# Optimization experiments

Measured on AMD Instinct MI355X. Metric: run time of the kernel, lower is better.

## Reference

```python
import jax, jax.numpy as jnp
import numpy as np

B, C, H, W = 16, 128, 32, 32
D, K = 64, 8192
BN_EPS = 1e-5
KLD_SCALE = 10.0
COMMIT = 0.25


def setup_inputs() -> dict:
    key = jax.random.key(0)
    ks = jax.random.split(key, 4)
    return {
        "z": jax.random.normal(ks[0], (B, C, H, W), dtype=jnp.float32),
        "proj_w": jax.random.normal(ks[1], (D, C), dtype=jnp.float32) * (1.0 / np.sqrt(C)),
        "proj_b": jax.random.normal(ks[2], (D,), dtype=jnp.float32) * 0.01,
        "gamma": jnp.ones((D,), dtype=jnp.float32),
        "beta": jnp.zeros((D,), dtype=jnp.float32),
        "running_mean": jnp.zeros((D,), dtype=jnp.float32),
        "running_var": jnp.ones((D,), dtype=jnp.float32),
        "embed": jax.random.normal(ks[3], (K, D), dtype=jnp.float32) * 0.1,
    }


def reference(z, proj_w, proj_b, gamma, beta, running_mean, running_var, embed):
    sg = jax.lax.stop_gradient
    b, c, h, w = z.shape
    # 1x1 conv projection: [B,C,H,W] -> [B,D,H,W]
    x = jnp.einsum('bchw,dc->bdhw', z, proj_w) + proj_b[None, :, None, None]
    # BatchNorm2d (inference mode: running stats)
    scale = gamma * jax.lax.rsqrt(running_var + BN_EPS)
    x = x * scale[None, :, None, None] + (beta - running_mean * scale)[None, :, None, None]
    # NCHW -> NHWC, flatten to [N, D]
    z_e = jnp.transpose(x, (0, 2, 3, 1))
    flat = z_e.reshape(-1, z_e.shape[-1])  # [N, D]
    # pairwise squared distances [N, K]
    dist = (jnp.sum(flat * flat, axis=1, keepdims=True)
            - 2.0 * flat @ embed.T
            + jnp.sum(embed * embed, axis=1)[None, :])
    ind = jnp.argmax(-dist, axis=1).reshape(b, h, w)  # [B,H,W]
    z_q = embed[ind]  # [B,H,W,D] codebook gather
    diff = KLD_SCALE * (COMMIT * jnp.mean((sg(z_q) - z_e) ** 2)
                        + jnp.mean((z_q - sg(z_e)) ** 2))
    z_q_st = z_e + sg(z_q - z_e)  # straight-through
    return jnp.transpose(z_q_st, (0, 3, 1, 2)), diff, ind
```

## Files before the change

### kernel.cpp

```cpp
#include <hip/hip_runtime.h>
#include <math.h>

#define B_   16
#define C_   128
#define H_   32
#define W_   32
#define D_   64
#define K_   8192
#define HW_  (H_*W_)
#define N_   (B_*HW_)

#define CS      16
#define CPB     (K_/CS)
#define CHUNK   128
#define NCH     (CPB/CHUNK)
#define ROWS_PB 256
#define MARGIN  0.12f
#define CAND_CAP 32

typedef short v8s __attribute__((ext_vector_type(8)));
typedef float v4f __attribute__((ext_vector_type(4)));

__device__ __forceinline__ short f2bf(float f) {
    union { float fv; unsigned u; } cv; cv.fv = f;
    unsigned u = cv.u;
    unsigned rnd = ((u >> 16) & 1u) + 0x7fffu;
    return (short)((u + rnd) >> 16);
}

#define GLOAD_LDS16(gp, lp) __builtin_amdgcn_global_load_lds( \
    (const __attribute__((address_space(1))) unsigned int*)(gp), \
    (__attribute__((address_space(3))) unsigned int*)(lp), 16, 0, 0)

__device__ __forceinline__ float exact_score(const float4* __restrict__ zr,
                                             const float* __restrict__ embed,
                                             float h, int k)
{
    const float4* ep = (const float4*)(embed + (size_t)k * D_);
    float sa = 0.f, sb = 0.f;
    #pragma unroll
    for (int d4 = 0; d4 < 16; d4 += 2) {
        float4 ea = ep[d4], eb = ep[d4 + 1];
        sa += ea.x*zr[d4].x + ea.y*zr[d4].y + ea.z*zr[d4].z + ea.w*zr[d4].w;
        sb += eb.x*zr[d4+1].x + eb.y*zr[d4+1].y + eb.z*zr[d4+1].z + eb.w*zr[d4+1].w;
    }
    return (sa + sb) - h;
}

__global__ __launch_bounds__(256) void k_proj(
    const float* __restrict__ z, const float* __restrict__ pw,
    const float* __restrict__ pb, const float* __restrict__ gamma,
    const float* __restrict__ beta, const float* __restrict__ rmean,
    const float* __restrict__ rvar, float* __restrict__ ze,
    short* __restrict__ zbf)
{
    __shared__ float zt[64][132];
    __shared__ float wl[64][132];
    const int tid = threadIdx.x;
    const int n0  = blockIdx.x * 64;
    const int b   = n0 / HW_;
    const int hw0 = n0 % HW_;
    const float* zb = z + (size_t)b * C_ * HW_ + hw0;

    #pragma unroll
    for (int it = 0; it < 32; ++it) {
        int flat = tid + 256 * it;
        int c = flat >> 6, p = flat & 63;
        zt[p][c] = zb[c * HW_ + p];
    }
    #pragma unroll
    for (int it = 0; it < 32; ++it) {
        int flat = tid + 256 * it;
        int d = flat >> 7, c = flat & 127;
        wl[d][c] = pw[d * C_ + c];
    }
    __syncthreads();

    const int tp = tid & 15;
    const int td = tid >> 4;
    float acc[4][4] = {};
    #pragma unroll
    for (int c4 = 0; c4 < 32; ++c4) {
        float4 zv[4], wv[4];
        #pragma unroll
        for (int i = 0; i < 4; ++i) zv[i] = *(const float4*)&zt[4*tp + i][4*c4];
        #pragma unroll
        for (int j = 0; j < 4; ++j) wv[j] = *(const float4*)&wl[4*td + j][4*c4];
        #pragma unroll
        for (int i = 0; i < 4; ++i)
            #pragma unroll
            for (int j = 0; j < 4; ++j)
                acc[i][j] += zv[i].x*wv[j].x + zv[i].y*wv[j].y
                           + zv[i].z*wv[j].z + zv[i].w*wv[j].w;
    }

    float sc[4], bi[4];
    #pragma unroll
    for (int j = 0; j < 4; ++j) {
        int d = 4*td + j;
        float s = gamma[d] / sqrtf(rvar[d] + 1e-5f);
        sc[j] = s;
        bi[j] = pb[d] * s + beta[d] - rmean[d] * s;
    }
    #pragma unroll
    for (int i = 0; i < 4; ++i) {
        int n = n0 + 4*tp + i;
        float4 o;
        o.x = acc[i][0]*sc[0] + bi[0];
        o.y = acc[i][1]*sc[1] + bi[1];
        o.z = acc[i][2]*sc[2] + bi[2];
        o.w = acc[i][3]*sc[3] + bi[3];
        *(float4*)&ze[(size_t)n * D_ + 4*td] = o;
        short4 ob;
        ob.x = f2bf(o.x); ob.y = f2bf(o.y); ob.z = f2bf(o.z); ob.w = f2bf(o.w);
        *(short4*)&zbf[(size_t)n * D_ + 4*td] = ob;
    }
}

__global__ __launch_bounds__(256) void k_prep(const float* __restrict__ e,
                                              float* __restrict__ hn,
                                              short* __restrict__ ebs)
{
    int t = blockIdx.x * 256 + threadIdx.x;
    float4 v = ((const float4*)e)[t];
    float s = v.x*v.x + v.y*v.y + v.z*v.z + v.w*v.w;
    s += __shfl_xor(s, 1);
    s += __shfl_xor(s, 2);
    s += __shfl_xor(s, 4);
    s += __shfl_xor(s, 8);
    if ((threadIdx.x & 15) == 0) hn[t >> 4] = 0.5f * s;

    const int k = t >> 4, p = t & 15;
    if (p < 8) {
        const int j = p ^ (k & 7);
        const float* src = e + (size_t)k * D_ + j * 8;
        v8s o;
        #pragma unroll
        for (int i = 0; i < 8; ++i) o[i] = f2bf(src[i]);
        *(v8s*)(ebs + (size_t)k * D_ + p * 8) = o;
    }
}

template<bool PUSH>
__global__ __launch_bounds__(256) void k_sweep(
    const short* __restrict__ zbf, const short* __restrict__ ebs,
    const float* __restrict__ hn, float* __restrict__ pbest,
    const float* __restrict__ Vm, int* __restrict__ cnt,
    int* __restrict__ cand)
{
    __shared__ short eb[2][CHUNK * 64];
    __shared__ float hl[2][CHUNK];
    const int tid  = threadIdx.x;
    const int lane = tid & 63;
    const int wv   = tid >> 6;
    const int q    = lane >> 4;
    const int l15  = lane & 15;
    const int m8   = l15 & 7;
    const int rowBase = blockIdx.x * ROWS_PB + wv * 64;
    const int code0   = blockIdx.y * CPB;

    v8s A[4][2];
    #pragma unroll
    for (int rt = 0; rt < 4; ++rt)
        #pragma unroll
        for (int f = 0; f < 2; ++f)
            A[rt][f] = *(const v8s*)(zbf + (size_t)(rowBase + rt*16 + l15) * D_
                                      + f*32 + q*8);

    float best[4][4];
    float vm[4][4];
    if (PUSH) {
        #pragma unroll
        for (int rt = 0; rt < 4; ++rt)
            #pragma unroll
            for (int r = 0; r < 4; ++r)
                vm[rt][r] = Vm[rowBase + rt*16 + q*4 + r];
    } else {
        #pragma unroll
        for (int rt = 0; rt < 4; ++rt)
            #pragma unroll
            for (int r = 0; r < 4; ++r) best[rt][r] = -INFINITY;
    }

    const int rb0 = l15 * 64 + ((q ^ m8) * 8);
    const int rb1 = l15 * 64 + (((q ^ m8) ^ 4) * 8);

    const char* srcBase = (const char*)(ebs + (size_t)code0 * 64);
    #define STAGE(b, ch) do {                                              \
        const char* s_ = srcBase + (size_t)(ch) * (CHUNK * 128);           \
        char* l_ = (char*)&eb[(b)][0];                                     \
        _Pragma("unroll")                                                  \
        for (int i_ = 0; i_ < 4; ++i_) {                                   \
            int seg_ = (wv * 4 + i_) * 1024 + lane * 16;                   \
            GLOAD_LDS16(s_ + seg_, l_ + seg_);                             \
        }                                                                  \
        if (tid < CHUNK) hl[(b)][tid] = hn[code0 + (ch) * CHUNK + tid];    \
    } while (0)

    STAGE(0, 0);
    __syncthreads();

    #pragma unroll 1
    for (int ch = 0; ch < NCH; ++ch) {
        const int buf = ch & 1;
        if (ch + 1 < NCH) STAGE(buf ^ 1, ch + 1);
        const int c0 = code0 + ch * CHUNK;
        const short* ep = &eb[buf][0];

        #pragma unroll
        for (int t = 0; t < CHUNK / 16; ++t) {
            v8s B0 = *(const v8s*)(ep + rb0 + t * 1024);
            v8s B1 = *(const v8s*)(ep + rb1 + t * 1024);
            const float mh = -hl[buf][t * 16 + l15];
            #pragma unroll
            for (int rt = 0; rt < 4; ++rt) {
                v4f c = {mh, mh, mh, mh};
                c = __builtin_amdgcn_mfma_f32_16x16x32_bf16(A[rt][0], B0, c, 0, 0, 0);
                c = __builtin_amdgcn_mfma_f32_16x16x32_bf16(A[rt][1], B1, c, 0, 0, 0);
                if (!PUSH) {
                    #pragma unroll
                    for (int r = 0; r < 4; ++r) best[rt][r] = fmaxf(best[rt][r], c[r]);
                } else {
                    bool a0 = c[0] > vm[rt][0];
                    bool a1 = c[1] > vm[rt][1];
                    bool a2 = c[2] > vm[rt][2];
                    bool a3 = c[3] > vm[rt][3];
                    if (a0 | a1 | a2 | a3) {
                        const int code = c0 + t * 16 + l15;
                        const int row0 = rowBase + rt*16 + q*4;
                        #pragma unroll
                        for (int r = 0; r < 4; ++r) {
                            if (c[r] > vm[rt][r]) {
                                int s = atomicAdd(&cnt[row0 + r], 1);
                                if (s < CAND_CAP) cand[(row0 + r) * CAND_CAP + s] = code;
                            }
                        }
                    }
                }
            }
        }
        __syncthreads();
    }
    #undef STAGE

    if (!PUSH) {
        #pragma unroll
        for (int rt = 0; rt < 4; ++rt)
            #pragma unroll
            for (int r = 0; r < 4; ++r) {
                float v = best[rt][r];
                v = fmaxf(v, __shfl_xor(v, 1));
                v = fmaxf(v, __shfl_xor(v, 2));
                v = fmaxf(v, __shfl_xor(v, 4));
                v = fmaxf(v, __shfl_xor(v, 8));
                if (l15 == 0)
                    pbest[(size_t)blockIdx.y * N_ + rowBase + rt*16 + q*4 + r] = v;
            }
    }
}

__global__ __launch_bounds__(256) void k_comb(const float* __restrict__ pbest,
                                              float* __restrict__ Vm,
                                              int* __restrict__ cnt)
{
    int n = blockIdx.x * 256 + threadIdx.x;
    float v = -INFINITY;
    #pragma unroll
    for (int s = 0; s < CS; ++s) v = fmaxf(v, pbest[(size_t)s * N_ + n]);
    Vm[n] = v - MARGIN;
    cnt[n] = 0;
}

__global__ __launch_bounds__(64) void k_pick(
    const int* __restrict__ cnt, const int* __restrict__ cand,
    const float* __restrict__ embed, const float* __restrict__ hn,
    const float* __restrict__ ze, float* __restrict__ out0,
    float* __restrict__ outIdx, float* __restrict__ bsum)
{
    const int tid = threadIdx.x;
    const int n   = blockIdx.x * 64 + tid;

    float4 zr[16];
    const float4* zp = (const float4*)(ze + (size_t)n * D_);
    #pragma unroll
    for (int i = 0; i < 16; ++i) zr[i] = zp[i];

    const int m = cnt[n];
    float best = -INFINITY;
    int   bidx = 0x7fffffff;
    if (m > CAND_CAP) {
        for (int k = 0; k < K_; ++k) {
            float s = exact_score(zr, embed, hn[k], k);
            if (s > best) { best = s; bidx = k; }
        }
    } else {
        for (int i = 0; i < m; ++i) {
            int k = cand[n * CAND_CAP + i];
            float s = exact_score(zr, embed, hn[k], k);
            if (s > best || (s == best && k < bidx)) { best = s; bidx = k; }
        }
    }
    if (bidx == 0x7fffffff) bidx = 0;
    outIdx[n] = (float)bidx;

    const float4* eq = (const float4*)(embed + (size_t)bidx * D_);
    const int b = n >> 10, hw = n & 1023;
    float* o = out0 + (size_t)b * (D_ * HW_) + hw;

    float local = 0.f;
    #pragma unroll
    for (int d4 = 0; d4 < 16; ++d4) {
        float4 e = eq[d4], zv = zr[d4];
        float dx = e.x - zv.x, dy = e.y - zv.y, dz = e.z - zv.z, dw = e.w - zv.w;
        local += dx*dx + dy*dy + dz*dz + dw*dw;
        o[(4*d4 + 0) * HW_] = e.x;
        o[(4*d4 + 1) * HW_] = e.y;
        o[(4*d4 + 2) * HW_] = e.z;
        o[(4*d4 + 3) * HW_] = e.w;
    }

    local += __shfl_xor(local, 1);
    local += __shfl_xor(local, 2);
    local += __shfl_xor(local, 4);
    local += __shfl_xor(local, 8);
    local += __shfl_xor(local, 16);
    local += __shfl_xor(local, 32);
    if (tid == 0) bsum[blockIdx.x] = local;
}

__global__ __launch_bounds__(256) void k_diff(const float* __restrict__ bsum,
                                              float* __restrict__ outd)
{
    __shared__ float red[256];
    float s = bsum[threadIdx.x];
    red[threadIdx.x] = s;
    __syncthreads();
    for (int st = 128; st > 0; st >>= 1) {
        if (threadIdx.x < st) red[threadIdx.x] += red[threadIdx.x + st];
        __syncthreads();
    }
    if (threadIdx.x == 0) *outd = red[0] * (12.5f / (float)(N_ * D_));
}

extern "C" void kernel_launch(void* const* d_in, const int* in_sizes, int n_in,
                              void* d_out, int out_size, void* d_ws, size_t ws_size,
                              hipStream_t stream)
{
    const float* z     = (const float*)d_in[0];
    const float* pw    = (const float*)d_in[1];
    const float* pb    = (const float*)d_in[2];
    const float* gamma = (const float*)d_in[3];
    const float* beta  = (const float*)d_in[4];
    const float* rmean = (const float*)d_in[5];
    const float* rvar  = (const float*)d_in[6];
    const float* embed = (const float*)d_in[7];

    float* out = (float*)d_out;
    float* out0    = out;
    float* outDiff = out + (size_t)N_ * D_;
    float* outIdx  = outDiff + 1;

    float* ws    = (float*)d_ws;
    float* ze    = ws;
    short* zbf   = (short*)(ze + (size_t)N_ * D_);
    short* ebs   = zbf + (size_t)N_ * D_;
    float* hn    = (float*)(ebs + (size_t)K_ * D_);
    float* pbest = hn + K_;
    float* Vm    = pbest + (size_t)CS * N_;
    int*   cnt   = (int*)(Vm + N_);
    int*   cand  = cnt + N_;
    float* bsum  = (float*)(cand + (size_t)N_ * CAND_CAP);

    k_proj <<<N_ / 64, 256, 0, stream>>>(z, pw, pb, gamma, beta, rmean, rvar, ze, zbf);
    k_prep <<<(K_ * 16) / 256, 256, 0, stream>>>(embed, hn, ebs);
    k_sweep<false><<<dim3(N_ / ROWS_PB, CS), 256, 0, stream>>>(
        zbf, ebs, hn, pbest, nullptr, nullptr, nullptr);
    k_comb <<<N_ / 256, 256, 0, stream>>>(pbest, Vm, cnt);
    k_sweep<true><<<dim3(N_ / ROWS_PB, CS), 256, 0, stream>>>(
        zbf, ebs, hn, pbest, Vm, cnt, cand);
    k_pick <<<N_ / 64, 64, 0, stream>>>(cnt, cand, embed, hn, ze, out0, outIdx, bsum);
    k_diff <<<1, 256, 0, stream>>>(bsum, outDiff);
}
```

Measured before the change: 170.4 us.

## Stream codebook fragments directly from global, merge prep kernels, drop diff reduction kernel

The sweep kernel no longer stages codebook chunks into LDS with global_load_lds and barriers. Each lane instead loads its own MFMA B fragments and norm straight from global/L2, with one-tile register prefetch. The projection and codebook-prep kernels are merged into a single launch, and the final diff reduction kernel is replaced by per-block atomicAdd into an output zeroed in k_comb. The goal is to cut launch count and barrier/LDS overhead, at the cost of more redundant global/L2 traffic (every wave reloads the same codebook), less latency hiding, and a non-deterministic float summation order for diff.

```diff
diff --git a/kernel.cpp b/kernel.cpp
--- a/kernel.cpp
+++ b/kernel.cpp
@@ -12,9 +12,7 @@
 
 #define CS      16
 #define CPB     (K_/CS)
-#define CHUNK   128
-#define NCH     (CPB/CHUNK)
-#define ROWS_PB 256
+#define NT      (CPB/16)
 #define MARGIN  0.12f
 #define CAND_CAP 32
 
@@ -28,10 +26,6 @@
     return (short)((u + rnd) >> 16);
 }
 
-#define GLOAD_LDS16(gp, lp) __builtin_amdgcn_global_load_lds( \
-    (const __attribute__((address_space(1))) unsigned int*)(gp), \
-    (__attribute__((address_space(3))) unsigned int*)(lp), 16, 0, 0)
-
 __device__ __forceinline__ float exact_score(const float4* __restrict__ zr,
                                              const float* __restrict__ embed,
                                              float h, int k)
@@ -47,16 +41,38 @@
     return (sa + sb) - h;
 }
 
-__global__ __launch_bounds__(256) void k_proj(
+__global__ __launch_bounds__(256) void k_projprep(
     const float* __restrict__ z, const float* __restrict__ pw,
     const float* __restrict__ pb, const float* __restrict__ gamma,
     const float* __restrict__ beta, const float* __restrict__ rmean,
-    const float* __restrict__ rvar, float* __restrict__ ze,
-    short* __restrict__ zbf)
+    const float* __restrict__ rvar, const float* __restrict__ embed,
+    float* __restrict__ ze, short* __restrict__ zbf,
+    short* __restrict__ ebs, float* __restrict__ hn)
 {
     __shared__ float zt[64][132];
     __shared__ float wl[64][132];
     const int tid = threadIdx.x;
+
+    if (blockIdx.x >= 256) {
+        int t = (blockIdx.x - 256) * 256 + tid;
+        float4 v = ((const float4*)embed)[t];
+        float s = v.x*v.x + v.y*v.y + v.z*v.z + v.w*v.w;
+        s += __shfl_xor(s, 1);
+        s += __shfl_xor(s, 2);
+        s += __shfl_xor(s, 4);
+        s += __shfl_xor(s, 8);
+        const int k = t >> 4, p = t & 15;
+        if (p == 0) hn[k] = 0.5f * s;
+        if (p < 8) {
+            const float* src = embed + (size_t)k * D_ + p * 8;
+            v8s o;
+            #pragma unroll
+            for (int i = 0; i < 8; ++i) o[i] = f2bf(src[i]);
+            *(v8s*)(ebs + (size_t)k * D_ + p * 8) = o;
+        }
+        return;
+    }
+
     const int n0  = blockIdx.x * 64;
     const int b   = n0 / HW_;
     const int hw0 = n0 % HW_;
@@ -117,30 +133,6 @@
     }
 }
 
-__global__ __launch_bounds__(256) void k_prep(const float* __restrict__ e,
-                                              float* __restrict__ hn,
-                                              short* __restrict__ ebs)
-{
-    int t = blockIdx.x * 256 + threadIdx.x;
-    float4 v = ((const float4*)e)[t];
-    float s = v.x*v.x + v.y*v.y + v.z*v.z + v.w*v.w;
-    s += __shfl_xor(s, 1);
-    s += __shfl_xor(s, 2);
-    s += __shfl_xor(s, 4);
-    s += __shfl_xor(s, 8);
-    if ((threadIdx.x & 15) == 0) hn[t >> 4] = 0.5f * s;
-
-    const int k = t >> 4, p = t & 15;
-    if (p < 8) {
-        const int j = p ^ (k & 7);
-        const float* src = e + (size_t)k * D_ + j * 8;
-        v8s o;
-        #pragma unroll
-        for (int i = 0; i < 8; ++i) o[i] = f2bf(src[i]);
-        *(v8s*)(ebs + (size_t)k * D_ + p * 8) = o;
-    }
-}
-
 template<bool PUSH>
 __global__ __launch_bounds__(256) void k_sweep(
     const short* __restrict__ zbf, const short* __restrict__ ebs,
@@ -148,15 +140,12 @@
     const float* __restrict__ Vm, int* __restrict__ cnt,
     int* __restrict__ cand)
 {
-    __shared__ short eb[2][CHUNK * 64];
-    __shared__ float hl[2][CHUNK];
     const int tid  = threadIdx.x;
     const int lane = tid & 63;
     const int wv   = tid >> 6;
     const int q    = lane >> 4;
     const int l15  = lane & 15;
-    const int m8   = l15 & 7;
-    const int rowBase = blockIdx.x * ROWS_PB + wv * 64;
+    const int rowBase = blockIdx.x * 256 + wv * 64;
     const int code0   = blockIdx.y * CPB;
 
     v8s A[4][2];
@@ -182,41 +171,31 @@
             for (int r = 0; r < 4; ++r) best[rt][r] = -INFINITY;
     }
 
-    const int rb0 = l15 * 64 + ((q ^ m8) * 8);
-    const int rb1 = l15 * 64 + (((q ^ m8) ^ 4) * 8);
-
-    const char* srcBase = (const char*)(ebs + (size_t)code0 * 64);
-    #define STAGE(b, ch) do {                                              \
-        const char* s_ = srcBase + (size_t)(ch) * (CHUNK * 128);           \
-        char* l_ = (char*)&eb[(b)][0];                                     \
-        _Pragma("unroll")                                                  \
-        for (int i_ = 0; i_ < 4; ++i_) {                                   \
-            int seg_ = (wv * 4 + i_) * 1024 + lane * 16;                   \
-            GLOAD_LDS16(s_ + seg_, l_ + seg_);                             \
-        }                                                                  \
-        if (tid < CHUNK) hl[(b)][tid] = hn[code0 + (ch) * CHUNK + tid];    \
-    } while (0)
-
-    STAGE(0, 0);
-    __syncthreads();
+    const short* pE = ebs + (size_t)(code0 + l15) * D_ + q * 8;
+    const float* pH = hn + code0 + l15;
+
+    v8s  cb0 = *(const v8s*)(pE);
+    v8s  cb1 = *(const v8s*)(pE + 32);
+    float chh = *pH;
 
     #pragma unroll 1
-    for (int ch = 0; ch < NCH; ++ch) {
-        const int buf = ch & 1;
-        if (ch + 1 < NCH) STAGE(buf ^ 1, ch + 1);
-        const int c0 = code0 + ch * CHUNK;
-        const short* ep = &eb[buf][0];
-
-        #pragma unroll
-        for (int t = 0; t < CHUNK / 16; ++t) {
-            v8s B0 = *(const v8s*)(ep + rb0 + t * 1024);
-            v8s B1 = *(const v8s*)(ep + rb1 + t * 1024);
-            const float mh = -hl[buf][t * 16 + l15];
+    for (int tc = 0; tc < 4; ++tc) {
+        #pragma unroll
+        for (int ti = 0; ti < 8; ++ti) {
+            const int t = tc * 8 + ti;
+            v8s nb0, nb1; float nhh;
+            const bool more = (t + 1 < NT);
+            if (more) {
+                nb0 = *(const v8s*)(pE + (t + 1) * 1024);
+                nb1 = *(const v8s*)(pE + (t + 1) * 1024 + 32);
+                nhh = pH[(t + 1) * 16];
+            }
+            const float mh = -chh;
             #pragma unroll
             for (int rt = 0; rt < 4; ++rt) {
                 v4f c = {mh, mh, mh, mh};
-                c = __builtin_amdgcn_mfma_f32_16x16x32_bf16(A[rt][0], B0, c, 0, 0, 0);
-                c = __builtin_amdgcn_mfma_f32_16x16x32_bf16(A[rt][1], B1, c, 0, 0, 0);
+                c = __builtin_amdgcn_mfma_f32_16x16x32_bf16(A[rt][0], cb0, c, 0, 0, 0);
+                c = __builtin_amdgcn_mfma_f32_16x16x32_bf16(A[rt][1], cb1, c, 0, 0, 0);
                 if (!PUSH) {
                     #pragma unroll
                     for (int r = 0; r < 4; ++r) best[rt][r] = fmaxf(best[rt][r], c[r]);
@@ -226,7 +205,7 @@
                     bool a2 = c[2] > vm[rt][2];
                     bool a3 = c[3] > vm[rt][3];
                     if (a0 | a1 | a2 | a3) {
-                        const int code = c0 + t * 16 + l15;
+                        const int code = code0 + t * 16 + l15;
                         const int row0 = rowBase + rt*16 + q*4;
                         #pragma unroll
                         for (int r = 0; r < 4; ++r) {
@@ -238,10 +217,9 @@
                     }
                 }
             }
+            if (more) { cb0 = nb0; cb1 = nb1; chh = nhh; }
         }
-        __syncthreads();
-    }
-    #undef STAGE
+    }
 
     if (!PUSH) {
         #pragma unroll
@@ -261,7 +239,8 @@
 
 __global__ __launch_bounds__(256) void k_comb(const float* __restrict__ pbest,
                                               float* __restrict__ Vm,
-                                              int* __restrict__ cnt)
+                                              int* __restrict__ cnt,
+                                              float* __restrict__ outDiff)
 {
     int n = blockIdx.x * 256 + threadIdx.x;
     float v = -INFINITY;
@@ -269,13 +248,14 @@
     for (int s = 0; s < CS; ++s) v = fmaxf(v, pbest[(size_t)s * N_ + n]);
     Vm[n] = v - MARGIN;
     cnt[n] = 0;
+    if (n == 0) *outDiff = 0.f;
 }
 
 __global__ __launch_bounds__(64) void k_pick(
     const int* __restrict__ cnt, const int* __restrict__ cand,
     const float* __restrict__ embed, const float* __restrict__ hn,
     const float* __restrict__ ze, float* __restrict__ out0,
-    float* __restrict__ outIdx, float* __restrict__ bsum)
+    float* __restrict__ outIdx, float* __restrict__ outDiff)
 {
     const int tid = threadIdx.x;
     const int n   = blockIdx.x * 64 + tid;
@@ -288,7 +268,7 @@
     const int m = cnt[n];
     float best = -INFINITY;
     int   bidx = 0x7fffffff;
-    if (m > CAND_CAP) {
+    if (m == 0 || m > CAND_CAP) {
         for (int k = 0; k < K_; ++k) {
             float s = exact_score(zr, embed, hn[k], k);
             if (s > best) { best = s; bidx = k; }
@@ -325,21 +305,7 @@
     local += __shfl_xor(local, 8);
     local += __shfl_xor(local, 16);
     local += __shfl_xor(local, 32);
-    if (tid == 0) bsum[blockIdx.x] = local;
-}
-
-__global__ __launch_bounds__(256) void k_diff(const float* __restrict__ bsum,
-                                              float* __restrict__ outd)
-{
-    __shared__ float red[256];
-    float s = bsum[threadIdx.x];
-    red[threadIdx.x] = s;
-    __syncthreads();
-    for (int st = 128; st > 0; st >>= 1) {
-        if (threadIdx.x < st) red[threadIdx.x] += red[threadIdx.x + st];
-        __syncthreads();
-    }
-    if (threadIdx.x == 0) *outd = red[0] * (12.5f / (float)(N_ * D_));
+    if (tid == 0) atomicAdd(outDiff, local * (12.5f / (float)(N_ * D_)));
 }
 
 extern "C" void kernel_launch(void* const* d_in, const int* in_sizes, int n_in,
@@ -369,15 +335,14 @@
     float* Vm    = pbest + (size_t)CS * N_;
     int*   cnt   = (int*)(Vm + N_);
     int*   cand  = cnt + N_;
-    float* bsum  = (float*)(cand + (size_t)N_ * CAND_CAP);
-
-    k_proj <<<N_ / 64, 256, 0, stream>>>(z, pw, pb, gamma, beta, rmean, rvar, ze, zbf);
-    k_prep <<<(K_ * 16) / 256, 256, 0, stream>>>(embed, hn, ebs);
-    k_sweep<false><<<dim3(N_ / ROWS_PB, CS), 256, 0, stream>>>(
+
+    k_projprep<<<256 + 512, 256, 0, stream>>>(z, pw, pb, gamma, beta, rmean,
+                                              rvar, embed, ze, zbf, ebs, hn);
+    k_sweep<false><<<dim3(N_ / 256, CS), 256, 0, stream>>>(
         zbf, ebs, hn, pbest, nullptr, nullptr, nullptr);
-    k_comb <<<N_ / 256, 256, 0, stream>>>(pbest, Vm, cnt);
-    k_sweep<true><<<dim3(N_ / ROWS_PB, CS), 256, 0, stream>>>(
+    k_comb <<<N_ / 256, 256, 0, stream>>>(pbest, Vm, cnt, outDiff);
+    k_sweep<true><<<dim3(N_ / 256, CS), 256, 0, stream>>>(
         zbf, ebs, hn, pbest, Vm, cnt, cand);
-    k_pick <<<N_ / 64, 64, 0, stream>>>(cnt, cand, embed, hn, ze, out0, outIdx, bsum);
-    k_diff <<<1, 256, 0, stream>>>(bsum, outDiff);
-}
+    k_pick <<<N_ / 64, 64, 0, stream>>>(cnt, cand, embed, hn, ze, out0,
+                                        outIdx, outDiff);
+}
```

New measurement: 211.5 us. 24.1% more time.
